# Kernel tuning notes

Measured on AMD Instinct MI355X. Metric: run time of the kernel, lower is better.

The kernel has to match this reference:

```python
import jax, jax.numpy as jnp
import numpy as np

B, T, D, N = 32, 2048, 1024, 1024  # batch, time, feature dim, n_dense


def setup_inputs() -> dict:
    key = jax.random.key(0)
    ks = jax.random.split(key, 8)
    s = 1.0 / np.sqrt(D)
    return {
        "query": jax.random.normal(ks[0], (B, D), jnp.float32),
        "values": jax.random.normal(ks[1], (B, T, D), jnp.float32),
        "W1": jax.random.uniform(ks[2], (D, N), jnp.float32, -s, s),
        "b1": jnp.zeros((N,), jnp.float32),
        "W2": jax.random.uniform(ks[3], (D, N), jnp.float32, -s, s),
        "b2": jnp.zeros((N,), jnp.float32),
        "V": jax.random.uniform(ks[4], (N, 1), jnp.float32, -1.0 / np.sqrt(N), 1.0 / np.sqrt(N)),
        "bV": jnp.zeros((1,), jnp.float32),
    }


def reference(query, values, W1, b1, W2, b2, V, bV):
    # q_proj: [B, 1, N], v_proj: [B, T, N]
    q_proj = (query @ W1 + b1)[:, None, :]
    v_proj = jnp.einsum("btd,dn->btn", values, W2) + b2
    # score: [B, T, 1]
    score = jnp.tanh(q_proj + v_proj) @ V + bV
    attention_weights = jax.nn.softmax(score, axis=1)  # softmax over time
    # context: [B, D]
    context_vector = jnp.sum(attention_weights * values, axis=1)
    return (context_vector, attention_weights)
```

## Files before the change

kernel.cpp:

```cpp
#include <hip/hip_runtime.h>
#include <hip/hip_bf16.h>

#define B_ 32
#define T_ 2048
#define D_ 1024
#define N_ 1024
#define M_ (B_*T_)

#define BM 64
#define BN 128
#define BK 64
#define NTSPLIT 2

typedef short bf16x8 __attribute__((ext_vector_type(8)));
typedef float f32x4 __attribute__((ext_vector_type(4)));
typedef unsigned short us4 __attribute__((ext_vector_type(4)));

__device__ __forceinline__ unsigned short bf16_rn(float x) {
    unsigned u = __float_as_uint(x);
    u += 0x7FFFu + ((u >> 16) & 1u);
    return (unsigned short)(u >> 16);
}

__device__ __forceinline__ void gload_lds16(const void* g, void* l) {
    __builtin_amdgcn_global_load_lds(
        (__attribute__((address_space(1))) void*)(g),
        (__attribute__((address_space(3))) void*)(l), 16, 0, 0);
}

__global__ void k0_w2t(const float* __restrict__ W2,
                       unsigned short* __restrict__ Th) {
    __shared__ float tile[32][33];
    int n0 = blockIdx.x * 32, d0 = blockIdx.y * 32;
    int tx = threadIdx.x & 31, ty = threadIdx.x >> 5;
    #pragma unroll
    for (int i = 0; i < 4; i++) {
        int d = d0 + ty + i * 8;
        tile[ty + i * 8][tx] = W2[d * N_ + n0 + tx];
    }
    __syncthreads();
    #pragma unroll
    for (int i = 0; i < 4; i++) {
        int n = n0 + ty + i * 8;
        Th[n * D_ + d0 + tx] = bf16_rn(tile[tx][ty + i * 8]);
    }
}

__global__ void k0_vals(const float* __restrict__ v,
                        unsigned short* __restrict__ o) {
    size_t i = ((size_t)blockIdx.x * 256 + threadIdx.x) * 8;
    const size_t stride = (size_t)gridDim.x * 256 * 8;
    for (; i < (size_t)M_ * D_; i += stride) {
        float4 a = *(const float4*)(v + i);
        float4 b = *(const float4*)(v + i + 4);
        us4 h0, h1;
        h0[0] = bf16_rn(a.x); h0[1] = bf16_rn(a.y);
        h0[2] = bf16_rn(a.z); h0[3] = bf16_rn(a.w);
        h1[0] = bf16_rn(b.x); h1[1] = bf16_rn(b.y);
        h1[2] = bf16_rn(b.z); h1[3] = bf16_rn(b.w);
        *(us4*)(o + i) = h0;
        *(us4*)(o + i + 4) = h1;
    }
}

__global__ void k1_qproj(const float* __restrict__ query,
                         const float* __restrict__ W1,
                         const float* __restrict__ b1,
                         float* __restrict__ qp) {
    int b = blockIdx.x;
    int n = blockIdx.y * 256 + threadIdx.x;
    const float* q = query + b * D_;
    const float* w = W1 + n;
    float s = 0.f;
    #pragma unroll 8
    for (int d = 0; d < D_; d++) s += q[d] * w[d * N_];
    qp[b * N_ + n] = s + b1[n];
}

__global__ __launch_bounds__(256, 2) void k2_score(
    const unsigned short* __restrict__ Av,
    const unsigned short* __restrict__ W2Th,
    const float* __restrict__ qp,
    const float* __restrict__ b2,
    const float* __restrict__ V,
    float* __restrict__ score) {
    __shared__ unsigned short sAh[BM * BK];
    __shared__ unsigned short sBh[BN * BK];
    __shared__ float red[2 * BM];

    const int tid = threadIdx.x;
    const int lane = tid & 63;
    const int wid = tid >> 6;
    const int wm = wid >> 1, wn = wid & 1;
    const int g = lane >> 4, c16 = lane & 15;

    const int bid = blockIdx.x;
    const int wgid = ((bid & 7) << 8) | (bid >> 3);
    const int m0 = (wgid >> 1) * BM;
    const int b = m0 >> 11;
    const int nt0 = (wgid & 1) * (N_ / BN / NTSPLIT);

    const int b_rl = lane >> 3;
    const int b_j = lane & 7;

    float rowpart[8];
    #pragma unroll
    for (int i = 0; i < 8; i++) rowpart[i] = 0.f;

    for (int nt = nt0; nt < nt0 + N_ / BN / NTSPLIT; nt++) {
        f32x4 acc[2][4];
        #pragma unroll
        for (int mi = 0; mi < 2; mi++)
            #pragma unroll
            for (int ni = 0; ni < 4; ni++) {
                f32x4 z = {0.f, 0.f, 0.f, 0.f};
                acc[mi][ni] = z;
            }

        for (int kt = 0; kt < D_ / BK; kt++) {
            const int k0 = kt * BK;
            __syncthreads();

            #pragma unroll
            for (int i = 0; i < 4; i++) {
                int r = wid * 32 + i * 8 + b_rl;
                int jj = b_j ^ (r & 7);
                size_t soff = (size_t)(nt * BN + r) * D_ + k0 + jj * 8;
                gload_lds16(W2Th + soff, &sBh[(wid * 32 + i * 8) * 64]);
            }
            #pragma unroll
            for (int i = 0; i < 2; i++) {
                int r = wid * 16 + i * 8 + b_rl;
                int jj = b_j ^ (r & 7);
                size_t soff = (size_t)(m0 + r) * D_ + k0 + jj * 8;
                gload_lds16(Av + soff, &sAh[(wid * 16 + i * 8) * 64]);
            }

            __syncthreads();

            #pragma unroll
            for (int s = 0; s < 2; s++) {
                bf16x8 aH[2], bH[4];
                #pragma unroll
                for (int mi = 0; mi < 2; mi++) {
                    int r = wm * 32 + mi * 16 + c16;
                    int idx = r * 64 + (((s * 4 + g) ^ (r & 7)) << 3);
                    aH[mi] = *(const bf16x8*)&sAh[idx];
                }
                #pragma unroll
                for (int ni = 0; ni < 4; ni++) {
                    int r = wn * 64 + ni * 16 + c16;
                    int idx = r * 64 + (((s * 4 + g) ^ (r & 7)) << 3);
                    bH[ni] = *(const bf16x8*)&sBh[idx];
                }
                #pragma unroll
                for (int mi = 0; mi < 2; mi++)
                    #pragma unroll
                    for (int ni = 0; ni < 4; ni++)
                        acc[mi][ni] = __builtin_amdgcn_mfma_f32_16x16x32_bf16(aH[mi], bH[ni], acc[mi][ni], 0, 0, 0);
            }
        }

        #pragma unroll
        for (int ni = 0; ni < 4; ni++) {
            int n = nt * BN + wn * 64 + ni * 16 + c16;
            float qv = qp[b * N_ + n] + b2[n];
            float Vv = V[n];
            #pragma unroll
            for (int mi = 0; mi < 2; mi++)
                #pragma unroll
                for (int r = 0; r < 4; r++) {
                    rowpart[mi * 4 + r] += tanhf(acc[mi][ni][r] + qv) * Vv;
                }
        }
    }

    #pragma unroll
    for (int i = 0; i < 8; i++) {
        float v = rowpart[i];
        v += __shfl_xor(v, 1);
        v += __shfl_xor(v, 2);
        v += __shfl_xor(v, 4);
        v += __shfl_xor(v, 8);
        rowpart[i] = v;
    }
    if (c16 == 0) {
        #pragma unroll
        for (int mi = 0; mi < 2; mi++)
            #pragma unroll
            for (int r = 0; r < 4; r++)
                red[wn * BM + wm * 32 + mi * 16 + g * 4 + r] = rowpart[mi * 4 + r];
    }
    __syncthreads();
    if (tid < BM) {
        atomicAdd(&score[m0 + tid], red[tid] + red[BM + tid]);
    }
}

__global__ void k3_softmax(float* __restrict__ sw) {
    int b = blockIdx.x;
    float* row = sw + b * T_;
    int tid = threadIdx.x;
    float v[8];
    float lmax = -1e30f;
    #pragma unroll
    for (int i = 0; i < 8; i++) {
        v[i] = row[tid + i * 256];
        lmax = fmaxf(lmax, v[i]);
    }
    #pragma unroll
    for (int d = 1; d < 64; d <<= 1) lmax = fmaxf(lmax, __shfl_xor(lmax, d));
    __shared__ float sm[4], ss[4];
    if ((tid & 63) == 0) sm[tid >> 6] = lmax;
    __syncthreads();
    lmax = fmaxf(fmaxf(sm[0], sm[1]), fmaxf(sm[2], sm[3]));
    float lsum = 0.f;
    #pragma unroll
    for (int i = 0; i < 8; i++) {
        v[i] = expf(v[i] - lmax);
        lsum += v[i];
    }
    #pragma unroll
    for (int d = 1; d < 64; d <<= 1) lsum += __shfl_xor(lsum, d);
    if ((tid & 63) == 0) ss[tid >> 6] = lsum;
    __syncthreads();
    lsum = ss[0] + ss[1] + ss[2] + ss[3];
    float inv = 1.f / lsum;
    #pragma unroll
    for (int i = 0; i < 8; i++) row[tid + i * 256] = v[i] * inv;
}

__global__ void k4_context(const unsigned short* __restrict__ Av,
                           const float* __restrict__ w,
                           float* __restrict__ ctx) {
    int b = blockIdx.x;
    int dc = blockIdx.y;
    int tc = blockIdx.z;
    int d4 = threadIdx.x & 31;
    int th = threadIdx.x >> 5;
    const float* wrow = w + b * T_;
    int d = dc * 128 + d4 * 4;
    const unsigned short* vbase = Av + (size_t)b * T_ * D_ + d;
    float4 acc = {0.f, 0.f, 0.f, 0.f};
    int t0 = tc * 256 + th * 32;
    for (int t = t0; t < t0 + 32; t++) {
        float wt = wrow[t];
        us4 hv = *(const us4*)(vbase + (size_t)t * D_);
        acc.x += wt * __uint_as_float((unsigned)hv[0] << 16);
        acc.y += wt * __uint_as_float((unsigned)hv[1] << 16);
        acc.z += wt * __uint_as_float((unsigned)hv[2] << 16);
        acc.w += wt * __uint_as_float((unsigned)hv[3] << 16);
    }
    __shared__ float4 red4[256];
    red4[threadIdx.x] = acc;
    __syncthreads();
    if (th == 0) {
        float4 s = red4[d4];
        #pragma unroll
        for (int i = 1; i < 8; i++) {
            float4 o = red4[i * 32 + d4];
            s.x += o.x; s.y += o.y; s.z += o.z; s.w += o.w;
        }
        atomicAdd(&ctx[b * D_ + d + 0], s.x);
        atomicAdd(&ctx[b * D_ + d + 1], s.y);
        atomicAdd(&ctx[b * D_ + d + 2], s.z);
        atomicAdd(&ctx[b * D_ + d + 3], s.w);
    }
}

extern "C" void kernel_launch(void* const* d_in, const int* in_sizes, int n_in,
                              void* d_out, int out_size, void* d_ws, size_t ws_size,
                              hipStream_t stream) {
    const float* query  = (const float*)d_in[0];
    const float* values = (const float*)d_in[1];
    const float* W1     = (const float*)d_in[2];
    const float* b1     = (const float*)d_in[3];
    const float* W2     = (const float*)d_in[4];
    const float* b2     = (const float*)d_in[5];
    const float* V      = (const float*)d_in[6];

    float* ctx = (float*)d_out;
    float* weights = (float*)d_out + B_ * D_;

    size_t need = (size_t)N_ * D_ * sizeof(unsigned short)
                + (size_t)B_ * N_ * sizeof(float)
                + (size_t)M_ * D_ * sizeof(unsigned short);
    if (ws_size < need) return;
    unsigned short* Th = (unsigned short*)d_ws;
    float* qp = (float*)(Th + (size_t)N_ * D_);
    unsigned short* Av = (unsigned short*)(qp + (size_t)B_ * N_);

    k0_w2t<<<dim3(N_ / 32, D_ / 32), 256, 0, stream>>>(W2, Th);
    k0_vals<<<2048, 256, 0, stream>>>(values, Av);
    k1_qproj<<<dim3(B_, N_ / 256), 256, 0, stream>>>(query, W1, b1, qp);
    hipMemsetAsync(weights, 0, (size_t)B_ * T_ * sizeof(float), stream);
    k2_score<<<(M_ / BM) * NTSPLIT, 256, 0, stream>>>(Av, Th, qp, b2, V, weights);
    k3_softmax<<<B_, 256, 0, stream>>>(weights);
    hipMemsetAsync(ctx, 0, (size_t)B_ * D_ * sizeof(float), stream);
    k4_context<<<dim3(B_, 8, 8), 256, 0, stream>>>(Av, weights, ctx);
}
```

Baseline: 358.6 us.

## Double-buffer LDS tiles in score GEMM and replace atomics with partial-score buffers

The score GEMM now uses two LDS buffers and a flattened n-tile/k-tile loop, issuing the global-to-LDS loads for the next step before computing on the current one, so only one barrier per step is needed. Atomic accumulation into the score output is replaced by writing each N-half's partial scores to a separate workspace buffer, which the softmax kernel sums; this also removes a memset. It doubles LDS use per block, which may lower occupancy.

```diff
diff --git a/kernel.cpp b/kernel.cpp
--- a/kernel.cpp
+++ b/kernel.cpp
@@ -11,6 +11,8 @@
 #define BN 128
 #define BK 64
 #define NTSPLIT 2
+#define NTP (N_ / BN / NTSPLIT)
+#define NSTEP (NTP * (D_ / BK))
 
 typedef short bf16x8 __attribute__((ext_vector_type(8)));
 typedef float f32x4 __attribute__((ext_vector_type(4)));
@@ -77,15 +79,37 @@
     qp[b * N_ + n] = s + b1[n];
 }
 
+__device__ __forceinline__ void k2_stage(int u, unsigned short* sa, unsigned short* sb,
+                                         int m0, int nt0, int wid, int b_rl, int b_j,
+                                         const unsigned short* __restrict__ Av,
+                                         const unsigned short* __restrict__ W2Th) {
+    const int nt = nt0 + (u >> 4);
+    const int k0 = (u & 15) * BK;
+    #pragma unroll
+    for (int i = 0; i < 4; i++) {
+        int r = wid * 32 + i * 8 + b_rl;
+        int jj = b_j ^ (r & 7);
+        size_t soff = (size_t)(nt * BN + r) * D_ + k0 + jj * 8;
+        gload_lds16(W2Th + soff, &sb[(wid * 32 + i * 8) * 64]);
+    }
+    #pragma unroll
+    for (int i = 0; i < 2; i++) {
+        int r = wid * 16 + i * 8 + b_rl;
+        int jj = b_j ^ (r & 7);
+        size_t soff = (size_t)(m0 + r) * D_ + k0 + jj * 8;
+        gload_lds16(Av + soff, &sa[(wid * 16 + i * 8) * 64]);
+    }
+}
+
 __global__ __launch_bounds__(256, 2) void k2_score(
     const unsigned short* __restrict__ Av,
     const unsigned short* __restrict__ W2Th,
     const float* __restrict__ qp,
     const float* __restrict__ b2,
     const float* __restrict__ V,
-    float* __restrict__ score) {
-    __shared__ unsigned short sAh[BM * BK];
-    __shared__ unsigned short sBh[BN * BK];
+    float* __restrict__ scorep) {
+    __shared__ unsigned short sA[2][BM * BK];
+    __shared__ unsigned short sB[2][BN * BK];
     __shared__ float red[2 * BM];
 
     const int tid = threadIdx.x;
@@ -98,7 +122,8 @@
     const int wgid = ((bid & 7) << 8) | (bid >> 3);
     const int m0 = (wgid >> 1) * BM;
     const int b = m0 >> 11;
-    const int nt0 = (wgid & 1) * (N_ / BN / NTSPLIT);
+    const int half = wgid & 1;
+    const int nt0 = half * NTP;
 
     const int b_rl = lane >> 3;
     const int b_j = lane & 7;
@@ -107,72 +132,69 @@
     #pragma unroll
     for (int i = 0; i < 8; i++) rowpart[i] = 0.f;
 
-    for (int nt = nt0; nt < nt0 + N_ / BN / NTSPLIT; nt++) {
-        f32x4 acc[2][4];
+    f32x4 acc[2][4];
+    #pragma unroll
+    for (int mi = 0; mi < 2; mi++)
         #pragma unroll
-        for (int mi = 0; mi < 2; mi++)
+        for (int ni = 0; ni < 4; ni++) {
+            f32x4 z = {0.f, 0.f, 0.f, 0.f};
+            acc[mi][ni] = z;
+        }
+
+    k2_stage(0, sA[0], sB[0], m0, nt0, wid, b_rl, b_j, Av, W2Th);
+    __syncthreads();
+
+    for (int u = 0; u < NSTEP; ++u) {
+        const int cur = u & 1;
+
+        if (u + 1 < NSTEP)
+            k2_stage(u + 1, sA[cur ^ 1], sB[cur ^ 1], m0, nt0, wid, b_rl, b_j, Av, W2Th);
+
+        #pragma unroll
+        for (int s = 0; s < 2; s++) {
+            bf16x8 aH[2], bH[4];
+            #pragma unroll
+            for (int mi = 0; mi < 2; mi++) {
+                int r = wm * 32 + mi * 16 + c16;
+                int idx = r * 64 + (((s * 4 + g) ^ (r & 7)) << 3);
+                aH[mi] = *(const bf16x8*)&sA[cur][idx];
+            }
             #pragma unroll
             for (int ni = 0; ni < 4; ni++) {
-                f32x4 z = {0.f, 0.f, 0.f, 0.f};
-                acc[mi][ni] = z;
+                int r = wn * 64 + ni * 16 + c16;
+                int idx = r * 64 + (((s * 4 + g) ^ (r & 7)) << 3);
+                bH[ni] = *(const bf16x8*)&sB[cur][idx];
             }
-
-        for (int kt = 0; kt < D_ / BK; kt++) {
-            const int k0 = kt * BK;
-            __syncthreads();
-
-            #pragma unroll
-            for (int i = 0; i < 4; i++) {
-                int r = wid * 32 + i * 8 + b_rl;
-                int jj = b_j ^ (r & 7);
-                size_t soff = (size_t)(nt * BN + r) * D_ + k0 + jj * 8;
-                gload_lds16(W2Th + soff, &sBh[(wid * 32 + i * 8) * 64]);
-            }
-            #pragma unroll
-            for (int i = 0; i < 2; i++) {
-                int r = wid * 16 + i * 8 + b_rl;
-                int jj = b_j ^ (r & 7);
-                size_t soff = (size_t)(m0 + r) * D_ + k0 + jj * 8;
-                gload_lds16(Av + soff, &sAh[(wid * 16 + i * 8) * 64]);
-            }
-
-            __syncthreads();
-
-            #pragma unroll
-            for (int s = 0; s < 2; s++) {
-                bf16x8 aH[2], bH[4];
+            #pragma unroll
+            for (int mi = 0; mi < 2; mi++)
                 #pragma unroll
-                for (int mi = 0; mi < 2; mi++) {
-                    int r = wm * 32 + mi * 16 + c16;
-                    int idx = r * 64 + (((s * 4 + g) ^ (r & 7)) << 3);
-                    aH[mi] = *(const bf16x8*)&sAh[idx];
-                }
-                #pragma unroll
-                for (int ni = 0; ni < 4; ni++) {
-                    int r = wn * 64 + ni * 16 + c16;
-                    int idx = r * 64 + (((s * 4 + g) ^ (r & 7)) << 3);
-                    bH[ni] = *(const bf16x8*)&sBh[idx];
-                }
+                for (int ni = 0; ni < 4; ni++)
+                    acc[mi][ni] = __builtin_amdgcn_mfma_f32_16x16x32_bf16(aH[mi], bH[ni], acc[mi][ni], 0, 0, 0);
+        }
+
+        if ((u & 15) == 15) {
+            int nt = nt0 + (u >> 4);
+            #pragma unroll
+            for (int ni = 0; ni < 4; ni++) {
+                int n = nt * BN + wn * 64 + ni * 16 + c16;
+                float qv = qp[b * N_ + n] + b2[n];
+                float Vv = V[n];
                 #pragma unroll
                 for (int mi = 0; mi < 2; mi++)
                     #pragma unroll
-                    for (int ni = 0; ni < 4; ni++)
-                        acc[mi][ni] = __builtin_amdgcn_mfma_f32_16x16x32_bf16(aH[mi], bH[ni], acc[mi][ni], 0, 0, 0);
+                    for (int r = 0; r < 4; r++)
+                        rowpart[mi * 4 + r] += tanhf(acc[mi][ni][r] + qv) * Vv;
             }
-        }
-
-        #pragma unroll
-        for (int ni = 0; ni < 4; ni++) {
-            int n = nt * BN + wn * 64 + ni * 16 + c16;
-            float qv = qp[b * N_ + n] + b2[n];
-            float Vv = V[n];
             #pragma unroll
             for (int mi = 0; mi < 2; mi++)
                 #pragma unroll
-                for (int r = 0; r < 4; r++) {
-                    rowpart[mi * 4 + r] += tanhf(acc[mi][ni][r] + qv) * Vv;
+                for (int ni = 0; ni < 4; ni++) {
+                    f32x4 z = {0.f, 0.f, 0.f, 0.f};
+                    acc[mi][ni] = z;
                 }
         }
+
+        __syncthreads();
     }
 
     #pragma unroll
@@ -193,19 +215,23 @@
     }
     __syncthreads();
     if (tid < BM) {
-        atomicAdd(&score[m0 + tid], red[tid] + red[BM + tid]);
-    }
-}
-
-__global__ void k3_softmax(float* __restrict__ sw) {
+        scorep[(size_t)half * M_ + m0 + tid] = red[tid] + red[BM + tid];
+    }
+}
+
+__global__ void k3_softmax(const float* __restrict__ sp,
+                           float* __restrict__ sw) {
     int b = blockIdx.x;
+    const float* r0 = sp + b * T_;
+    const float* r1 = sp + M_ + b * T_;
     float* row = sw + b * T_;
     int tid = threadIdx.x;
     float v[8];
     float lmax = -1e30f;
     #pragma unroll
     for (int i = 0; i < 8; i++) {
-        v[i] = row[tid + i * 256];
+        int idx = tid + i * 256;
+        v[i] = r0[idx] + r1[idx];
         lmax = fmaxf(lmax, v[i]);
     }
     #pragma unroll
@@ -284,18 +310,19 @@
 
     size_t need = (size_t)N_ * D_ * sizeof(unsigned short)
                 + (size_t)B_ * N_ * sizeof(float)
+                + (size_t)NTSPLIT * M_ * sizeof(float)
                 + (size_t)M_ * D_ * sizeof(unsigned short);
     if (ws_size < need) return;
     unsigned short* Th = (unsigned short*)d_ws;
     float* qp = (float*)(Th + (size_t)N_ * D_);
-    unsigned short* Av = (unsigned short*)(qp + (size_t)B_ * N_);
+    float* scorep = qp + (size_t)B_ * N_;
+    unsigned short* Av = (unsigned short*)(scorep + (size_t)NTSPLIT * M_);
 
     k0_w2t<<<dim3(N_ / 32, D_ / 32), 256, 0, stream>>>(W2, Th);
     k0_vals<<<2048, 256, 0, stream>>>(values, Av);
     k1_qproj<<<dim3(B_, N_ / 256), 256, 0, stream>>>(query, W1, b1, qp);
-    hipMemsetAsync(weights, 0, (size_t)B_ * T_ * sizeof(float), stream);
-    k2_score<<<(M_ / BM) * NTSPLIT, 256, 0, stream>>>(Av, Th, qp, b2, V, weights);
-    k3_softmax<<<B_, 256, 0, stream>>>(weights);
+    k2_score<<<(M_ / BM) * NTSPLIT, 256, 0, stream>>>(Av, Th, qp, b2, V, scorep);
+    k3_softmax<<<B_, 256, 0, stream>>>(scorep, weights);
     hipMemsetAsync(ctx, 0, (size_t)B_ * D_ * sizeof(float), stream);
     k4_context<<<dim3(B_, 8, 8), 256, 0, stream>>>(Av, weights, ctx);
 }
```

After: 395.7 us. 1.1x slower.

## Merge prep kernels into one launch and replace score atomics with split partial buffers

Applied to the files above, without the earlier changes.

Folds the three preprocessing kernels (values bf16 cast, W2 transpose, query projection) into a single block-dispatched kernel. The score kernel now writes each N-half's partial score to its own buffer instead of atomically adding into a zeroed output, and the softmax kernel sums the two halves. This removes two kernel launches, a memset and the atomics, at the cost of an extra workspace buffer and a little more read traffic in the softmax.

```diff
diff --git a/kernel.cpp b/kernel.cpp
--- a/kernel.cpp
+++ b/kernel.cpp
@@ -11,6 +11,7 @@
 #define BN 128
 #define BK 64
 #define NTSPLIT 2
+#define NTP (N_ / BN / NTSPLIT)
 
 typedef short bf16x8 __attribute__((ext_vector_type(8)));
 typedef float f32x4 __attribute__((ext_vector_type(4)));
@@ -28,53 +29,55 @@
         (__attribute__((address_space(3))) void*)(l), 16, 0, 0);
 }
 
-__global__ void k0_w2t(const float* __restrict__ W2,
-                       unsigned short* __restrict__ Th) {
+__global__ void k_prep(const float* __restrict__ values, unsigned short* __restrict__ Av,
+                       const float* __restrict__ W2, unsigned short* __restrict__ Th,
+                       const float* __restrict__ query, const float* __restrict__ W1,
+                       const float* __restrict__ b1, float* __restrict__ qp) {
     __shared__ float tile[32][33];
-    int n0 = blockIdx.x * 32, d0 = blockIdx.y * 32;
-    int tx = threadIdx.x & 31, ty = threadIdx.x >> 5;
-    #pragma unroll
-    for (int i = 0; i < 4; i++) {
-        int d = d0 + ty + i * 8;
-        tile[ty + i * 8][tx] = W2[d * N_ + n0 + tx];
-    }
-    __syncthreads();
-    #pragma unroll
-    for (int i = 0; i < 4; i++) {
-        int n = n0 + ty + i * 8;
-        Th[n * D_ + d0 + tx] = bf16_rn(tile[tx][ty + i * 8]);
-    }
-}
-
-__global__ void k0_vals(const float* __restrict__ v,
-                        unsigned short* __restrict__ o) {
-    size_t i = ((size_t)blockIdx.x * 256 + threadIdx.x) * 8;
-    const size_t stride = (size_t)gridDim.x * 256 * 8;
-    for (; i < (size_t)M_ * D_; i += stride) {
-        float4 a = *(const float4*)(v + i);
-        float4 b = *(const float4*)(v + i + 4);
-        us4 h0, h1;
-        h0[0] = bf16_rn(a.x); h0[1] = bf16_rn(a.y);
-        h0[2] = bf16_rn(a.z); h0[3] = bf16_rn(a.w);
-        h1[0] = bf16_rn(b.x); h1[1] = bf16_rn(b.y);
-        h1[2] = bf16_rn(b.z); h1[3] = bf16_rn(b.w);
-        *(us4*)(o + i) = h0;
-        *(us4*)(o + i + 4) = h1;
-    }
-}
-
-__global__ void k1_qproj(const float* __restrict__ query,
-                         const float* __restrict__ W1,
-                         const float* __restrict__ b1,
-                         float* __restrict__ qp) {
-    int b = blockIdx.x;
-    int n = blockIdx.y * 256 + threadIdx.x;
-    const float* q = query + b * D_;
-    const float* w = W1 + n;
-    float s = 0.f;
-    #pragma unroll 8
-    for (int d = 0; d < D_; d++) s += q[d] * w[d * N_];
-    qp[b * N_ + n] = s + b1[n];
+    const int blk = blockIdx.x;
+    const int tid = threadIdx.x;
+
+    if (blk < 2048) {
+        size_t base = (size_t)blk * 32768 + (size_t)tid * 8;
+        #pragma unroll 4
+        for (int it = 0; it < 16; ++it) {
+            size_t i = base + (size_t)it * 2048;
+            float4 a = *(const float4*)(values + i);
+            float4 b = *(const float4*)(values + i + 4);
+            us4 h0, h1;
+            h0[0] = bf16_rn(a.x); h0[1] = bf16_rn(a.y);
+            h0[2] = bf16_rn(a.z); h0[3] = bf16_rn(a.w);
+            h1[0] = bf16_rn(b.x); h1[1] = bf16_rn(b.y);
+            h1[2] = bf16_rn(b.z); h1[3] = bf16_rn(b.w);
+            *(us4*)(Av + i) = h0;
+            *(us4*)(Av + i + 4) = h1;
+        }
+    } else if (blk < 3072) {
+        int t = blk - 2048;
+        int n0 = (t & 31) * 32, d0 = (t >> 5) * 32;
+        int tx = tid & 31, ty = tid >> 5;
+        #pragma unroll
+        for (int i = 0; i < 4; i++) {
+            int d = d0 + ty + i * 8;
+            tile[ty + i * 8][tx] = W2[d * N_ + n0 + tx];
+        }
+        __syncthreads();
+        #pragma unroll
+        for (int i = 0; i < 4; i++) {
+            int n = n0 + ty + i * 8;
+            Th[n * D_ + d0 + tx] = bf16_rn(tile[tx][ty + i * 8]);
+        }
+    } else {
+        int t = blk - 3072;
+        int b = t & 31;
+        int n = (t >> 5) * 256 + tid;
+        const float* q = query + b * D_;
+        const float* w = W1 + n;
+        float s = 0.f;
+        #pragma unroll 8
+        for (int d = 0; d < D_; d++) s += q[d] * w[d * N_];
+        qp[b * N_ + n] = s + b1[n];
+    }
 }
 
 __global__ __launch_bounds__(256, 2) void k2_score(
@@ -83,7 +86,7 @@
     const float* __restrict__ qp,
     const float* __restrict__ b2,
     const float* __restrict__ V,
-    float* __restrict__ score) {
+    float* __restrict__ scorep) {
     __shared__ unsigned short sAh[BM * BK];
     __shared__ unsigned short sBh[BN * BK];
     __shared__ float red[2 * BM];
@@ -98,7 +101,8 @@
     const int wgid = ((bid & 7) << 8) | (bid >> 3);
     const int m0 = (wgid >> 1) * BM;
     const int b = m0 >> 11;
-    const int nt0 = (wgid & 1) * (N_ / BN / NTSPLIT);
+    const int half = wgid & 1;
+    const int nt0 = half * NTP;
 
     const int b_rl = lane >> 3;
     const int b_j = lane & 7;
@@ -107,7 +111,7 @@
     #pragma unroll
     for (int i = 0; i < 8; i++) rowpart[i] = 0.f;
 
-    for (int nt = nt0; nt < nt0 + N_ / BN / NTSPLIT; nt++) {
+    for (int nt = nt0; nt < nt0 + NTP; nt++) {
         f32x4 acc[2][4];
         #pragma unroll
         for (int mi = 0; mi < 2; mi++)
@@ -193,19 +197,23 @@
     }
     __syncthreads();
     if (tid < BM) {
-        atomicAdd(&score[m0 + tid], red[tid] + red[BM + tid]);
-    }
-}
-
-__global__ void k3_softmax(float* __restrict__ sw) {
+        scorep[(size_t)half * M_ + m0 + tid] = red[tid] + red[BM + tid];
+    }
+}
+
+__global__ void k3_softmax(const float* __restrict__ sp,
+                           float* __restrict__ sw) {
     int b = blockIdx.x;
+    const float* r0 = sp + b * T_;
+    const float* r1 = sp + M_ + b * T_;
     float* row = sw + b * T_;
     int tid = threadIdx.x;
     float v[8];
     float lmax = -1e30f;
     #pragma unroll
     for (int i = 0; i < 8; i++) {
-        v[i] = row[tid + i * 256];
+        int idx = tid + i * 256;
+        v[i] = r0[idx] + r1[idx];
         lmax = fmaxf(lmax, v[i]);
     }
     #pragma unroll
@@ -284,18 +292,17 @@
 
     size_t need = (size_t)N_ * D_ * sizeof(unsigned short)
                 + (size_t)B_ * N_ * sizeof(float)
+                + (size_t)NTSPLIT * M_ * sizeof(float)
                 + (size_t)M_ * D_ * sizeof(unsigned short);
     if (ws_size < need) return;
     unsigned short* Th = (unsigned short*)d_ws;
     float* qp = (float*)(Th + (size_t)N_ * D_);
-    unsigned short* Av = (unsigned short*)(qp + (size_t)B_ * N_);
-
-    k0_w2t<<<dim3(N_ / 32, D_ / 32), 256, 0, stream>>>(W2, Th);
-    k0_vals<<<2048, 256, 0, stream>>>(values, Av);
-    k1_qproj<<<dim3(B_, N_ / 256), 256, 0, stream>>>(query, W1, b1, qp);
-    hipMemsetAsync(weights, 0, (size_t)B_ * T_ * sizeof(float), stream);
-    k2_score<<<(M_ / BM) * NTSPLIT, 256, 0, stream>>>(Av, Th, qp, b2, V, weights);
-    k3_softmax<<<B_, 256, 0, stream>>>(weights);
+    float* scorep = qp + (size_t)B_ * N_;
+    unsigned short* Av = (unsigned short*)(scorep + (size_t)NTSPLIT * M_);
+
+    k_prep<<<3200, 256, 0, stream>>>(values, Av, W2, Th, query, W1, b1, qp);
+    k2_score<<<(M_ / BM) * NTSPLIT, 256, 0, stream>>>(Av, Th, qp, b2, V, scorep);
+    k3_softmax<<<B_, 256, 0, stream>>>(scorep, weights);
     hipMemsetAsync(ctx, 0, (size_t)B_ * D_ * sizeof(float), stream);
     k4_context<<<dim3(B_, 8, 8), 256, 0, stream>>>(Av, weights, ctx);
 }
```

Result: faster. 347.0 us (-3.2%).
